# Performance work log

Hardware: AMD Instinct MI355X
Metric: run time of the kernel (lower is better)

Reference implementation:

```python
import jax, jax.numpy as jnp
import numpy as np

N_HEADS = 8
HEAD_DIM = 32
KSIZE = 3
IN_CH = 128
OUT_CH = 256


def setup_inputs() -> dict:
    key = jax.random.key(0)
    k1, k2, k3, k4 = jax.random.split(key, 4)
    x = jax.random.normal(k1, (8, IN_CH, 64, 64), dtype=jnp.float32)
    w_key = jax.random.normal(k2, (N_HEADS * HEAD_DIM, IN_CH), dtype=jnp.float32) * 0.05
    b_key = jax.random.normal(k3, (N_HEADS * HEAD_DIM,), dtype=jnp.float32) * 0.05
    # memory init in torch: uniform in [-1, 1)
    memory = jax.random.uniform(k4, (N_HEADS, HEAD_DIM * KSIZE * KSIZE, OUT_CH // N_HEADS),
                                dtype=jnp.float32) * 2.0 - 1.0
    return {"x": x, "w_key": w_key, "b_key": b_key, "memory": memory}


def _unfold(z, k):
    # z: [b, C, Hp, Wp] padded; returns [b, C*k*k, H*W] with torch.unfold layout
    b, C, Hp, Wp = z.shape
    H, W = Hp - k + 1, Wp - k + 1
    patches = [z[:, :, i:i + H, j:j + W] for i in range(k) for j in range(k)]
    # stack -> [b, C, k*k, H, W]; channel-major like torch unfold (C outer, kh*k+kw inner)
    p = jnp.stack(patches, axis=2)
    return p.reshape(b, C * k * k, H * W)


def reference(x, w_key, b_key, memory):
    b, c_in, H, W = x.shape
    k = KSIZE
    m = N_HEADS
    # 1x1 conv (to_mem_key)
    key_map = jnp.einsum('oi,bihw->bohw', w_key, x) + b_key[None, :, None, None]
    # ZeroPad2d((k//2, k%2, k//2, k%2)) = (left, right, top, bottom)
    pl, pr = k // 2, k % 2
    padded = jnp.pad(key_map, ((0, 0), (0, 0), (pl, pr), (pl, pr)))
    unf = _unfold(padded, k)                      # [b, C*k*k, L], C = m*head_dim
    ckk = unf.shape[1]
    L = unf.shape[2]
    c = ckk // m
    # rearrange 'b (c m) l -> b m c l' (m is the FAST factor, per einops pattern)
    attn = unf.reshape(b, c, m, L).transpose(0, 2, 1, 3)   # [b, m, c, L]
    attn = jax.nn.softmax(attn, axis=2)
    out = jnp.einsum('nki,bnkl->bnil', memory, attn)       # [b, m, head_out, L]
    # rearrange 'b m c (h w) -> b (m c) h w'
    return out.reshape(b, m * out.shape[2], H, W)
```

## Files before the change

### kernel.cpp

```cpp
#include <hip/hip_runtime.h>
#include <hip/hip_bf16.h>

#define B_   8
#define CIN  128
#define CKEY 256
#define NH   8
#define HOUT 32
#define CPH  288
#define HW   4096

#define ESTR   264
#define EROW   (66 * ESTR)
#define E2_BYTES   (4 * EROW * 2)
#define XBUF_BYTES (64 * 136 * 2)
#define SMEM_BYTES (E2_BYTES + XBUF_BYTES)

typedef __attribute__((ext_vector_type(8))) short bf16x8;
typedef __attribute__((ext_vector_type(4))) float f32x4;

static __device__ __forceinline__ unsigned bfpack2(float a, float b) {
  __hip_bfloat162 h = __float22bfloat162_rn(float2{a, b});
  unsigned r;
  __builtin_memcpy(&r, &h, 4);
  return r;
}

__global__ __launch_bounds__(512, 2) void fused_kernel(
    const float* __restrict__ x, const float* __restrict__ wk,
    const float* __restrict__ mem, const float* __restrict__ bk,
    float* __restrict__ out)
{
  extern __shared__ char smem[];
  unsigned short* e2 = (unsigned short*)smem;
  unsigned*       xdw = (unsigned*)(smem + E2_BYTES);

  const int tid = threadIdx.x;
  const int bid = blockIdx.x;
  const int b  = bid & 7;
  const int h0 = (bid >> 3) * 2;
  const int lane = tid & 63;
  const int wv = __builtin_amdgcn_readfirstlane(tid >> 6);
  const int li = lane & 15, q = lane >> 4;

  float bias[2][4];
#pragma unroll
  for (int sh = 0; sh < 2; ++sh)
#pragma unroll
    for (int r = 0; r < 4; ++r)
      bias[sh][r] = bk[wv + 8 * (sh * 16 + 4 * q + r)];

  const int spx = tid & 63, sicg = tid >> 6;
  const int sxor = ((spx >> 3) & 7) << 3;

  const bool valid[4] = {h0 - 1 >= 0, true, true, h0 + 2 < 64};
  unsigned pk[4][8];
#pragma unroll
  for (int r = 0; r < 4; ++r) {
    if (!valid[r]) continue;
    const int y = h0 - 1 + r;
    const float* xr = x + (size_t)b * CIN * HW + y * 64 + spx;
#pragma unroll
    for (int r4 = 0; r4 < 4; ++r4) {
      const int ic0 = 4 * sicg + 32 * r4;
      const float v0 = xr[(size_t)(ic0 + 0) * HW];
      const float v1 = xr[(size_t)(ic0 + 1) * HW];
      const float v2 = xr[(size_t)(ic0 + 2) * HW];
      const float v3 = xr[(size_t)(ic0 + 3) * HW];
      pk[r][2 * r4 + 0] = bfpack2(v0, v1);
      pk[r][2 * r4 + 1] = bfpack2(v2, v3);
    }
  }

  bf16x8 wf[2][4];
#pragma unroll
  for (int sh = 0; sh < 2; ++sh)
#pragma unroll
    for (int ks = 0; ks < 4; ++ks) {
      const int och = wv + 8 * (sh * 16 + li);
      const float* src = wk + (size_t)och * CIN + ks * 32 + q * 8;
      const float4 v0 = *(const float4*)(src);
      const float4 v1 = *(const float4*)(src + 4);
      const int4 piv = make_int4(bfpack2(v0.x, v0.y), bfpack2(v0.z, v0.w),
                                 bfpack2(v1.x, v1.y), bfpack2(v1.z, v1.w));
      wf[sh][ks] = __builtin_bit_cast(bf16x8, piv);
    }

  bf16x8 mfr[9][2];
#pragma unroll
  for (int p = 0; p < 9; ++p) {
    const int cb = (wv - p + 8) & 7;
#pragma unroll
    for (int ib = 0; ib < 2; ++ib) {
      const int i = ib * 16 + li;
      unsigned pr[4];
#pragma unroll
      for (int jj = 0; jj < 4; ++jj) {
        const int s0 = q * 8 + 2 * jj;
        const int c0 = cb + 8 * s0;
        const int c1 = cb + 8 * (s0 + 1);
        const int t0 = (9 * c0 + p) >> 3;
        const int t1 = (9 * c1 + p) >> 3;
        const float f0 = mem[((size_t)wv * CPH + t0) * HOUT + i];
        const float f1 = mem[((size_t)wv * CPH + t1) * HOUT + i];
        pr[jj] = bfpack2(f0, f1);
      }
      mfr[p][ib] = __builtin_bit_cast(bf16x8, make_int4(pr[0], pr[1], pr[2], pr[3]));
    }
  }

#pragma unroll
  for (int r = 0; r < 4; r += 3) {
    if (!valid[r]) {
      unsigned* erow = (unsigned*)(e2 + r * EROW);
      for (int d = tid; d < 66 * 132; d += 512) erow[d] = 0x3F803F80u;
    }
  }

#pragma unroll
  for (int rr = 0; rr < 4; ++rr) {
    if (valid[rr]) {
#pragma unroll
      for (int r4 = 0; r4 < 4; ++r4) {
        const int o = (2 * sicg + 16 * r4) ^ sxor;
        *(uint2*)(xdw + spx * 68 + o) = make_uint2(pk[rr][2 * r4], pk[rr][2 * r4 + 1]);
      }
    }
    __syncthreads();
    if (valid[rr]) {
      f32x4 acc[2][4];
#pragma unroll
      for (int sh = 0; sh < 2; ++sh)
#pragma unroll
        for (int pt = 0; pt < 4; ++pt) {
          f32x4 cv; cv[0] = bias[sh][0]; cv[1] = bias[sh][1];
          cv[2] = bias[sh][2]; cv[3] = bias[sh][3];
          acc[sh][pt] = cv;
        }
#pragma unroll
      for (int ks = 0; ks < 4; ++ks) {
        const bf16x8 a0 = wf[0][ks];
        const bf16x8 a1 = wf[1][ks];
#pragma unroll
        for (int pt = 0; pt < 4; ++pt) {
          const int px  = pt * 16 + li;
          const int blk = (ks * 16 + q * 4) ^ (((px >> 3) & 7) << 3);
          const bf16x8 bfr = *(const bf16x8*)(xdw + px * 68 + blk);
          acc[0][pt] = __builtin_amdgcn_mfma_f32_16x16x32_bf16(a0, bfr, acc[0][pt], 0, 0, 0);
          acc[1][pt] = __builtin_amdgcn_mfma_f32_16x16x32_bf16(a1, bfr, acc[1][pt], 0, 0, 0);
        }
      }
      unsigned short* erow = e2 + rr * EROW;
#pragma unroll
      for (int sh = 0; sh < 2; ++sh)
#pragma unroll
        for (int pt = 0; pt < 4; ++pt) {
          const float w0 = __expf(acc[sh][pt][0]);
          const float w1 = __expf(acc[sh][pt][1]);
          const float w2 = __expf(acc[sh][pt][2]);
          const float w3 = __expf(acc[sh][pt][3]);
          unsigned short* dst = erow + (pt * 16 + li + 1) * ESTR
                              + wv * 32 + sh * 16 + 4 * q;
          *(uint2*)dst = make_uint2(bfpack2(w0, w1), bfpack2(w2, w3));
        }
      if (tid < 256) {
        const int xcol = (tid & 1) ? 65 : 0;
        ((unsigned*)(erow + xcol * ESTR))[tid >> 1] = 0x3F803F80u;
      }
    }
    __syncthreads();
  }

  const int m = wv;
  const int4 onesi = make_int4(0x3F803F80, 0x3F803F80, 0x3F803F80, 0x3F803F80);
  const bf16x8 bones = __builtin_bit_cast(bf16x8, onesi);

#pragma unroll
  for (int hh = 0; hh < 2; ++hh) {
    f32x4 acc[4][2], accs[4];
#pragma unroll
    for (int pb = 0; pb < 4; ++pb) {
      acc[pb][0] = {0.f, 0.f, 0.f, 0.f};
      acc[pb][1] = {0.f, 0.f, 0.f, 0.f};
      accs[pb]   = {0.f, 0.f, 0.f, 0.f};
    }
#pragma unroll
    for (int p = 0; p < 9; ++p) {
      const bf16x8 bm0 = mfr[p][0];
      const bf16x8 bm1 = mfr[p][1];
      const int cm   = (m - p + 8) & 7;
      const int rrow = hh + p / 3;
      const int dxp  = p - 3 * (p / 3);
      const unsigned short* abase = e2 + rrow * EROW + (li + dxp) * ESTR
                                  + cm * 32 + q * 8;
#pragma unroll
      for (int pb = 0; pb < 4; ++pb) {
        const bf16x8 af = *(const bf16x8*)(abase + pb * 16 * ESTR);
        acc[pb][0] = __builtin_amdgcn_mfma_f32_16x16x32_bf16(bm0, af, acc[pb][0], 0, 0, 0);
        acc[pb][1] = __builtin_amdgcn_mfma_f32_16x16x32_bf16(bm1, af, acc[pb][1], 0, 0, 0);
        accs[pb]   = __builtin_amdgcn_mfma_f32_16x16x32_bf16(bones, af, accs[pb], 0, 0, 0);
      }
    }
    float* ob = out + ((size_t)(b * CKEY + m * HOUT)) * HW + (h0 + hh) * 64;
#pragma unroll
    for (int pb = 0; pb < 4; ++pb) {
      const float inv = 1.0f / accs[pb][0];
#pragma unroll
      for (int n = 0; n < 2; ++n)
#pragma unroll
        for (int r = 0; r < 4; ++r)
          ob[(size_t)(n * 16 + 4 * q + r) * HW + pb * 16 + li] =
              acc[pb][n][r] * inv;
    }
  }
}

extern "C" void kernel_launch(void* const* d_in, const int* in_sizes, int n_in,
                              void* d_out, int out_size, void* d_ws, size_t ws_size,
                              hipStream_t stream) {
  const float* x   = (const float*)d_in[0];
  const float* wk  = (const float*)d_in[1];
  const float* bk  = (const float*)d_in[2];
  const float* mem = (const float*)d_in[3];
  (void)d_ws; (void)ws_size;

  (void)hipFuncSetAttribute((const void*)fused_kernel,
                            hipFuncAttributeMaxDynamicSharedMemorySize, SMEM_BYTES);

  fused_kernel<<<dim3(256), dim3(512), SMEM_BYTES, stream>>>(
      x, wk, mem, bk, (float*)d_out);
}
```

Baseline: 110.9 us.

## Split fused kernel into conv+exp kernel and attention kernel via global workspace

Replaces the single fused kernel, which recomputed the 1x1 conv for halo rows (4 rows per 2 output rows), with two kernels. The first computes exp(conv) for each row once into a padded bf16 global buffer and also prepacks the memory MFMA fragments. The second reads the three neighbouring rows from global memory to do the softmax-weighted aggregation, one output row per block. This removes the duplicated conv work and the large LDS footprint, at the cost of an extra launch and a global round trip of about 17 MB of bf16 intermediates.

```diff
diff --git a/kernel.cpp b/kernel.cpp
--- a/kernel.cpp
+++ b/kernel.cpp
@@ -9,11 +9,11 @@
 #define CPH  288
 #define HW   4096
 
-#define ESTR   264
-#define EROW   (66 * ESTR)
-#define E2_BYTES   (4 * EROW * 2)
-#define XBUF_BYTES (64 * 136 * 2)
-#define SMEM_BYTES (E2_BYTES + XBUF_BYTES)
+#define EPX   256
+#define EROWG (66 * EPX)
+#define EBATG (66 * EROWG)
+#define E_BYTES   ((size_t)B_ * EBATG * 2)
+#define MFRAG_OFF E_BYTES
 
 typedef __attribute__((ext_vector_type(8))) short bf16x8;
 typedef __attribute__((ext_vector_type(4))) float f32x4;
@@ -24,23 +24,46 @@
   __builtin_memcpy(&r, &h, 4);
   return r;
 }
-
-__global__ __launch_bounds__(512, 2) void fused_kernel(
+static __device__ __forceinline__ unsigned short f2bf(float f) {
+  unsigned u = __builtin_bit_cast(unsigned, f);
+  u += 0x7FFFu + ((u >> 16) & 1u);
+  return (unsigned short)(u >> 16);
+}
+
+__global__ __launch_bounds__(512, 2) void conv_kernel(
     const float* __restrict__ x, const float* __restrict__ wk,
-    const float* __restrict__ mem, const float* __restrict__ bk,
-    float* __restrict__ out)
+    const float* __restrict__ bk, const float* __restrict__ mem,
+    unsigned short* __restrict__ EG, unsigned short* __restrict__ mfragP)
 {
-  extern __shared__ char smem[];
-  unsigned short* e2 = (unsigned short*)smem;
-  unsigned*       xdw = (unsigned*)(smem + E2_BYTES);
-
+  __shared__ unsigned xdw[64 * 68];
   const int tid = threadIdx.x;
-  const int bid = blockIdx.x;
-  const int b  = bid & 7;
-  const int h0 = (bid >> 3) * 2;
+  const int gb = blockIdx.x;
+
+  if (gb >= 512) {
+    const int idx  = (gb - 512) * 512 + tid;
+    const int lane = idx & 63, fi = idx >> 6;
+    const int ib = fi & 1, pm = fi >> 1;
+    const int p = pm % 9, mh = pm / 9;
+    const int li = lane & 15, q = lane >> 4;
+    const int i = ib * 16 + li;
+    unsigned short* dst = mfragP + (size_t)idx * 8;
+#pragma unroll
+    for (int j = 0; j < 8; ++j) {
+      const int s = q * 8 + j;
+      const int c = ((mh - p + 8) & 7) + 8 * s;
+      const int t = (9 * c + p) >> 3;
+      dst[j] = f2bf(mem[((size_t)mh * CPH + t) * HOUT + i]);
+    }
+    return;
+  }
+
+  const int b = gb & 7;
+  const int y = gb >> 3;
   const int lane = tid & 63;
   const int wv = __builtin_amdgcn_readfirstlane(tid >> 6);
   const int li = lane & 15, q = lane >> 4;
+  const int spx = tid & 63, sicg = tid >> 6;
+  const int sxor = ((spx >> 3) & 7) << 3;
 
   float bias[2][4];
 #pragma unroll
@@ -49,26 +72,17 @@
     for (int r = 0; r < 4; ++r)
       bias[sh][r] = bk[wv + 8 * (sh * 16 + 4 * q + r)];
 
-  const int spx = tid & 63, sicg = tid >> 6;
-  const int sxor = ((spx >> 3) & 7) << 3;
-
-  const bool valid[4] = {h0 - 1 >= 0, true, true, h0 + 2 < 64};
-  unsigned pk[4][8];
-#pragma unroll
-  for (int r = 0; r < 4; ++r) {
-    if (!valid[r]) continue;
-    const int y = h0 - 1 + r;
-    const float* xr = x + (size_t)b * CIN * HW + y * 64 + spx;
-#pragma unroll
-    for (int r4 = 0; r4 < 4; ++r4) {
-      const int ic0 = 4 * sicg + 32 * r4;
-      const float v0 = xr[(size_t)(ic0 + 0) * HW];
-      const float v1 = xr[(size_t)(ic0 + 1) * HW];
-      const float v2 = xr[(size_t)(ic0 + 2) * HW];
-      const float v3 = xr[(size_t)(ic0 + 3) * HW];
-      pk[r][2 * r4 + 0] = bfpack2(v0, v1);
-      pk[r][2 * r4 + 1] = bfpack2(v2, v3);
-    }
+  unsigned pk[8];
+  const float* xr = x + (size_t)b * CIN * HW + y * 64 + spx;
+#pragma unroll
+  for (int r4 = 0; r4 < 4; ++r4) {
+    const int ic0 = 4 * sicg + 32 * r4;
+    const float v0 = xr[(size_t)(ic0 + 0) * HW];
+    const float v1 = xr[(size_t)(ic0 + 1) * HW];
+    const float v2 = xr[(size_t)(ic0 + 2) * HW];
+    const float v3 = xr[(size_t)(ic0 + 3) * HW];
+    pk[2 * r4 + 0] = bfpack2(v0, v1);
+    pk[2 * r4 + 1] = bfpack2(v2, v3);
   }
 
   bf16x8 wf[2][4];
@@ -85,132 +99,117 @@
       wf[sh][ks] = __builtin_bit_cast(bf16x8, piv);
     }
 
-  bf16x8 mfr[9][2];
-#pragma unroll
-  for (int p = 0; p < 9; ++p) {
-    const int cb = (wv - p + 8) & 7;
-#pragma unroll
-    for (int ib = 0; ib < 2; ++ib) {
-      const int i = ib * 16 + li;
-      unsigned pr[4];
-#pragma unroll
-      for (int jj = 0; jj < 4; ++jj) {
-        const int s0 = q * 8 + 2 * jj;
-        const int c0 = cb + 8 * s0;
-        const int c1 = cb + 8 * (s0 + 1);
-        const int t0 = (9 * c0 + p) >> 3;
-        const int t1 = (9 * c1 + p) >> 3;
-        const float f0 = mem[((size_t)wv * CPH + t0) * HOUT + i];
-        const float f1 = mem[((size_t)wv * CPH + t1) * HOUT + i];
-        pr[jj] = bfpack2(f0, f1);
-      }
-      mfr[p][ib] = __builtin_bit_cast(bf16x8, make_int4(pr[0], pr[1], pr[2], pr[3]));
-    }
-  }
-
-#pragma unroll
-  for (int r = 0; r < 4; r += 3) {
-    if (!valid[r]) {
-      unsigned* erow = (unsigned*)(e2 + r * EROW);
-      for (int d = tid; d < 66 * 132; d += 512) erow[d] = 0x3F803F80u;
-    }
-  }
-
-#pragma unroll
-  for (int rr = 0; rr < 4; ++rr) {
-    if (valid[rr]) {
-#pragma unroll
-      for (int r4 = 0; r4 < 4; ++r4) {
-        const int o = (2 * sicg + 16 * r4) ^ sxor;
-        *(uint2*)(xdw + spx * 68 + o) = make_uint2(pk[rr][2 * r4], pk[rr][2 * r4 + 1]);
-      }
-    }
-    __syncthreads();
-    if (valid[rr]) {
-      f32x4 acc[2][4];
-#pragma unroll
-      for (int sh = 0; sh < 2; ++sh)
-#pragma unroll
-        for (int pt = 0; pt < 4; ++pt) {
-          f32x4 cv; cv[0] = bias[sh][0]; cv[1] = bias[sh][1];
-          cv[2] = bias[sh][2]; cv[3] = bias[sh][3];
-          acc[sh][pt] = cv;
-        }
-#pragma unroll
-      for (int ks = 0; ks < 4; ++ks) {
-        const bf16x8 a0 = wf[0][ks];
-        const bf16x8 a1 = wf[1][ks];
-#pragma unroll
-        for (int pt = 0; pt < 4; ++pt) {
-          const int px  = pt * 16 + li;
-          const int blk = (ks * 16 + q * 4) ^ (((px >> 3) & 7) << 3);
-          const bf16x8 bfr = *(const bf16x8*)(xdw + px * 68 + blk);
-          acc[0][pt] = __builtin_amdgcn_mfma_f32_16x16x32_bf16(a0, bfr, acc[0][pt], 0, 0, 0);
-          acc[1][pt] = __builtin_amdgcn_mfma_f32_16x16x32_bf16(a1, bfr, acc[1][pt], 0, 0, 0);
-        }
-      }
-      unsigned short* erow = e2 + rr * EROW;
-#pragma unroll
-      for (int sh = 0; sh < 2; ++sh)
-#pragma unroll
-        for (int pt = 0; pt < 4; ++pt) {
-          const float w0 = __expf(acc[sh][pt][0]);
-          const float w1 = __expf(acc[sh][pt][1]);
-          const float w2 = __expf(acc[sh][pt][2]);
-          const float w3 = __expf(acc[sh][pt][3]);
-          unsigned short* dst = erow + (pt * 16 + li + 1) * ESTR
-                              + wv * 32 + sh * 16 + 4 * q;
-          *(uint2*)dst = make_uint2(bfpack2(w0, w1), bfpack2(w2, w3));
-        }
-      if (tid < 256) {
-        const int xcol = (tid & 1) ? 65 : 0;
-        ((unsigned*)(erow + xcol * ESTR))[tid >> 1] = 0x3F803F80u;
-      }
-    }
-    __syncthreads();
-  }
-
-  const int m = wv;
+#pragma unroll
+  for (int r4 = 0; r4 < 4; ++r4) {
+    const int o = (2 * sicg + 16 * r4) ^ sxor;
+    *(uint2*)(xdw + spx * 68 + o) = make_uint2(pk[2 * r4], pk[2 * r4 + 1]);
+  }
+  __syncthreads();
+
+  f32x4 acc[2][4];
+#pragma unroll
+  for (int sh = 0; sh < 2; ++sh)
+#pragma unroll
+    for (int pt = 0; pt < 4; ++pt) {
+      f32x4 cv; cv[0] = bias[sh][0]; cv[1] = bias[sh][1];
+      cv[2] = bias[sh][2]; cv[3] = bias[sh][3];
+      acc[sh][pt] = cv;
+    }
+#pragma unroll
+  for (int ks = 0; ks < 4; ++ks) {
+    const bf16x8 a0 = wf[0][ks];
+    const bf16x8 a1 = wf[1][ks];
+#pragma unroll
+    for (int pt = 0; pt < 4; ++pt) {
+      const int px  = pt * 16 + li;
+      const int blk = (ks * 16 + q * 4) ^ (((px >> 3) & 7) << 3);
+      const bf16x8 bfr = *(const bf16x8*)(xdw + px * 68 + blk);
+      acc[0][pt] = __builtin_amdgcn_mfma_f32_16x16x32_bf16(a0, bfr, acc[0][pt], 0, 0, 0);
+      acc[1][pt] = __builtin_amdgcn_mfma_f32_16x16x32_bf16(a1, bfr, acc[1][pt], 0, 0, 0);
+    }
+  }
+
+  unsigned short* erow = EG + (size_t)(b * 66 + y + 1) * EROWG;
+#pragma unroll
+  for (int sh = 0; sh < 2; ++sh)
+#pragma unroll
+    for (int pt = 0; pt < 4; ++pt) {
+      const float w0 = __expf(acc[sh][pt][0]);
+      const float w1 = __expf(acc[sh][pt][1]);
+      const float w2 = __expf(acc[sh][pt][2]);
+      const float w3 = __expf(acc[sh][pt][3]);
+      unsigned short* dst = erow + (size_t)(pt * 16 + li + 1) * EPX
+                          + wv * 32 + sh * 16 + 4 * q;
+      *(uint2*)dst = make_uint2(bfpack2(w0, w1), bfpack2(w2, w3));
+    }
+
+  unsigned* rowdw = (unsigned*)erow;
+  if (tid < 256) {
+    const int c = tid & 127;
+    if (tid < 128) rowdw[c] = 0x3F803F80u;
+    else           rowdw[65 * 128 + c] = 0x3F803F80u;
+  }
+  if (y == 0) {
+    unsigned* r0 = (unsigned*)(EG + (size_t)(b * 66 + 0) * EROWG);
+    for (int d = tid; d < 66 * 128; d += 512) r0[d] = 0x3F803F80u;
+  }
+  if (y == 63) {
+    unsigned* r65 = (unsigned*)(EG + (size_t)(b * 66 + 65) * EROWG);
+    for (int d = tid; d < 66 * 128; d += 512) r65[d] = 0x3F803F80u;
+  }
+}
+
+__global__ __launch_bounds__(512, 2) void attn_kernel(
+    const unsigned short* __restrict__ EG,
+    const unsigned short* __restrict__ mfragP,
+    float* __restrict__ out)
+{
+  const int tid = threadIdx.x, bid = blockIdx.x;
+  const int b = bid & 7, h = bid >> 3;
+  const int lane = tid & 63;
+  const int m = __builtin_amdgcn_readfirstlane(tid >> 6);
+  const int li = lane & 15, q = lane >> 4;
+
+  const unsigned short* mf = mfragP + (size_t)(m * 9) * 2 * 64 * 8;
   const int4 onesi = make_int4(0x3F803F80, 0x3F803F80, 0x3F803F80, 0x3F803F80);
   const bf16x8 bones = __builtin_bit_cast(bf16x8, onesi);
 
-#pragma unroll
-  for (int hh = 0; hh < 2; ++hh) {
-    f32x4 acc[4][2], accs[4];
+  f32x4 acc[4][2], accs[4];
+#pragma unroll
+  for (int pb = 0; pb < 4; ++pb) {
+    acc[pb][0] = {0.f, 0.f, 0.f, 0.f};
+    acc[pb][1] = {0.f, 0.f, 0.f, 0.f};
+    accs[pb]   = {0.f, 0.f, 0.f, 0.f};
+  }
+
+#pragma unroll
+  for (int p = 0; p < 9; ++p) {
+    const bf16x8 bm0 = *(const bf16x8*)(mf + ((size_t)((p * 2 + 0) * 64 + lane)) * 8);
+    const bf16x8 bm1 = *(const bf16x8*)(mf + ((size_t)((p * 2 + 1) * 64 + lane)) * 8);
+    const int cm  = (m - p + 8) & 7;
+    const int ry  = h + p / 3;
+    const int dxp = p - 3 * (p / 3);
+    const unsigned short* abase = EG + (size_t)(b * 66 + ry) * EROWG
+                                + (size_t)(li + dxp) * EPX + cm * 32 + q * 8;
 #pragma unroll
     for (int pb = 0; pb < 4; ++pb) {
-      acc[pb][0] = {0.f, 0.f, 0.f, 0.f};
-      acc[pb][1] = {0.f, 0.f, 0.f, 0.f};
-      accs[pb]   = {0.f, 0.f, 0.f, 0.f};
-    }
-#pragma unroll
-    for (int p = 0; p < 9; ++p) {
-      const bf16x8 bm0 = mfr[p][0];
-      const bf16x8 bm1 = mfr[p][1];
-      const int cm   = (m - p + 8) & 7;
-      const int rrow = hh + p / 3;
-      const int dxp  = p - 3 * (p / 3);
-      const unsigned short* abase = e2 + rrow * EROW + (li + dxp) * ESTR
-                                  + cm * 32 + q * 8;
-#pragma unroll
-      for (int pb = 0; pb < 4; ++pb) {
-        const bf16x8 af = *(const bf16x8*)(abase + pb * 16 * ESTR);
-        acc[pb][0] = __builtin_amdgcn_mfma_f32_16x16x32_bf16(bm0, af, acc[pb][0], 0, 0, 0);
-        acc[pb][1] = __builtin_amdgcn_mfma_f32_16x16x32_bf16(bm1, af, acc[pb][1], 0, 0, 0);
-        accs[pb]   = __builtin_amdgcn_mfma_f32_16x16x32_bf16(bones, af, accs[pb], 0, 0, 0);
-      }
-    }
-    float* ob = out + ((size_t)(b * CKEY + m * HOUT)) * HW + (h0 + hh) * 64;
-#pragma unroll
-    for (int pb = 0; pb < 4; ++pb) {
-      const float inv = 1.0f / accs[pb][0];
-#pragma unroll
-      for (int n = 0; n < 2; ++n)
-#pragma unroll
-        for (int r = 0; r < 4; ++r)
-          ob[(size_t)(n * 16 + 4 * q + r) * HW + pb * 16 + li] =
-              acc[pb][n][r] * inv;
-    }
+      const bf16x8 af = *(const bf16x8*)(abase + (size_t)pb * 16 * EPX);
+      acc[pb][0] = __builtin_amdgcn_mfma_f32_16x16x32_bf16(bm0, af, acc[pb][0], 0, 0, 0);
+      acc[pb][1] = __builtin_amdgcn_mfma_f32_16x16x32_bf16(bm1, af, acc[pb][1], 0, 0, 0);
+      accs[pb]   = __builtin_amdgcn_mfma_f32_16x16x32_bf16(bones, af, accs[pb], 0, 0, 0);
+    }
+  }
+
+  float* ob = out + ((size_t)(b * CKEY + m * HOUT)) * HW + h * 64;
+#pragma unroll
+  for (int pb = 0; pb < 4; ++pb) {
+    const float inv = 1.0f / accs[pb][0];
+#pragma unroll
+    for (int n = 0; n < 2; ++n)
+#pragma unroll
+      for (int r = 0; r < 4; ++r)
+        ob[(size_t)(n * 16 + 4 * q + r) * HW + pb * 16 + li] =
+            acc[pb][n][r] * inv;
   }
 }
 
@@ -221,11 +220,10 @@
   const float* wk  = (const float*)d_in[1];
   const float* bk  = (const float*)d_in[2];
   const float* mem = (const float*)d_in[3];
-  (void)d_ws; (void)ws_size;
-
-  (void)hipFuncSetAttribute((const void*)fused_kernel,
-                            hipFuncAttributeMaxDynamicSharedMemorySize, SMEM_BYTES);
-
-  fused_kernel<<<dim3(256), dim3(512), SMEM_BYTES, stream>>>(
-      x, wk, mem, bk, (float*)d_out);
-}
+
+  unsigned short* EG     = (unsigned short*)d_ws;
+  unsigned short* mfragP = (unsigned short*)((char*)d_ws + MFRAG_OFF);
+
+  conv_kernel<<<dim3(530), dim3(512), 0, stream>>>(x, wk, bk, mem, EG, mfragP);
+  attn_kernel<<<dim3(512), dim3(512), 0, stream>>>(EG, mfragP, (float*)d_out);
+}
```

New measurement: 111.9 us. About the same (+0.9%).

## Use 1024-thread blocks splitting heads/rows across waves and prepack memory fragments

Applied to the files above, without the earlier changes.

Doubles the block size to 16 waves so each wave handles one head and one half (key-map channel half, then one output row), halving per-wave register state. The memory-matrix bf16 MFMA fragments are built once by a small prep kernel into workspace, so each block no longer gathers and converts them with scattered loads. This adds a second kernel launch and global fragment loads in the main loop. Occupancy changes from two 512-thread blocks per CU to one 1024-thread block.

```diff
diff --git a/kernel.cpp b/kernel.cpp
--- a/kernel.cpp
+++ b/kernel.cpp
@@ -24,10 +24,34 @@
   __builtin_memcpy(&r, &h, 4);
   return r;
 }
-
-__global__ __launch_bounds__(512, 2) void fused_kernel(
+static __device__ __forceinline__ unsigned short f2bf(float f) {
+  unsigned u = __builtin_bit_cast(unsigned, f);
+  u += 0x7FFFu + ((u >> 16) & 1u);
+  return (unsigned short)(u >> 16);
+}
+
+__global__ __launch_bounds__(256) void prep_kernel(
+    const float* __restrict__ mem, unsigned short* __restrict__ mfragP)
+{
+  const int idx  = blockIdx.x * 256 + threadIdx.x;
+  const int lane = idx & 63, fi = idx >> 6;
+  const int ib = fi & 1, pm = fi >> 1;
+  const int p = pm % 9, m = pm / 9;
+  const int li = lane & 15, q = lane >> 4;
+  const int i = ib * 16 + li;
+  unsigned short* dst = mfragP + (size_t)idx * 8;
+#pragma unroll
+  for (int j = 0; j < 8; ++j) {
+    const int s = q * 8 + j;
+    const int c = ((m - p + 8) & 7) + 8 * s;
+    const int t = (9 * c + p) >> 3;
+    dst[j] = f2bf(mem[((size_t)m * CPH + t) * HOUT + i]);
+  }
+}
+
+__global__ __launch_bounds__(1024) void fused_kernel(
     const float* __restrict__ x, const float* __restrict__ wk,
-    const float* __restrict__ mem, const float* __restrict__ bk,
+    const unsigned short* __restrict__ mfragP, const float* __restrict__ bk,
     float* __restrict__ out)
 {
   extern __shared__ char smem[];
@@ -40,79 +64,53 @@
   const int h0 = (bid >> 3) * 2;
   const int lane = tid & 63;
   const int wv = __builtin_amdgcn_readfirstlane(tid >> 6);
+  const int cm = wv & 7, sh = wv >> 3;
   const int li = lane & 15, q = lane >> 4;
 
-  float bias[2][4];
-#pragma unroll
-  for (int sh = 0; sh < 2; ++sh)
-#pragma unroll
-    for (int r = 0; r < 4; ++r)
-      bias[sh][r] = bk[wv + 8 * (sh * 16 + 4 * q + r)];
-
-  const int spx = tid & 63, sicg = tid >> 6;
+  float bias[4];
+#pragma unroll
+  for (int r = 0; r < 4; ++r)
+    bias[r] = bk[cm + 8 * (sh * 16 + 4 * q + r)];
+
+  const int spx = tid & 63, g = tid >> 6;
   const int sxor = ((spx >> 3) & 7) << 3;
 
   const bool valid[4] = {h0 - 1 >= 0, true, true, h0 + 2 < 64};
-  unsigned pk[4][8];
+  unsigned pk[4][4];
 #pragma unroll
   for (int r = 0; r < 4; ++r) {
     if (!valid[r]) continue;
     const int y = h0 - 1 + r;
     const float* xr = x + (size_t)b * CIN * HW + y * 64 + spx;
 #pragma unroll
-    for (int r4 = 0; r4 < 4; ++r4) {
-      const int ic0 = 4 * sicg + 32 * r4;
+    for (int r2 = 0; r2 < 2; ++r2) {
+      const int ic0 = 4 * g + 64 * r2;
       const float v0 = xr[(size_t)(ic0 + 0) * HW];
       const float v1 = xr[(size_t)(ic0 + 1) * HW];
       const float v2 = xr[(size_t)(ic0 + 2) * HW];
       const float v3 = xr[(size_t)(ic0 + 3) * HW];
-      pk[r][2 * r4 + 0] = bfpack2(v0, v1);
-      pk[r][2 * r4 + 1] = bfpack2(v2, v3);
-    }
-  }
-
-  bf16x8 wf[2][4];
-#pragma unroll
-  for (int sh = 0; sh < 2; ++sh)
-#pragma unroll
-    for (int ks = 0; ks < 4; ++ks) {
-      const int och = wv + 8 * (sh * 16 + li);
-      const float* src = wk + (size_t)och * CIN + ks * 32 + q * 8;
-      const float4 v0 = *(const float4*)(src);
-      const float4 v1 = *(const float4*)(src + 4);
-      const int4 piv = make_int4(bfpack2(v0.x, v0.y), bfpack2(v0.z, v0.w),
-                                 bfpack2(v1.x, v1.y), bfpack2(v1.z, v1.w));
-      wf[sh][ks] = __builtin_bit_cast(bf16x8, piv);
-    }
-
-  bf16x8 mfr[9][2];
-#pragma unroll
-  for (int p = 0; p < 9; ++p) {
-    const int cb = (wv - p + 8) & 7;
-#pragma unroll
-    for (int ib = 0; ib < 2; ++ib) {
-      const int i = ib * 16 + li;
-      unsigned pr[4];
-#pragma unroll
-      for (int jj = 0; jj < 4; ++jj) {
-        const int s0 = q * 8 + 2 * jj;
-        const int c0 = cb + 8 * s0;
-        const int c1 = cb + 8 * (s0 + 1);
-        const int t0 = (9 * c0 + p) >> 3;
-        const int t1 = (9 * c1 + p) >> 3;
-        const float f0 = mem[((size_t)wv * CPH + t0) * HOUT + i];
-        const float f1 = mem[((size_t)wv * CPH + t1) * HOUT + i];
-        pr[jj] = bfpack2(f0, f1);
-      }
-      mfr[p][ib] = __builtin_bit_cast(bf16x8, make_int4(pr[0], pr[1], pr[2], pr[3]));
-    }
+      pk[r][2 * r2 + 0] = bfpack2(v0, v1);
+      pk[r][2 * r2 + 1] = bfpack2(v2, v3);
+    }
+  }
+
+  bf16x8 wf[4];
+#pragma unroll
+  for (int ks = 0; ks < 4; ++ks) {
+    const int och = cm + 8 * (sh * 16 + li);
+    const float* src = wk + (size_t)och * CIN + ks * 32 + q * 8;
+    const float4 v0 = *(const float4*)(src);
+    const float4 v1 = *(const float4*)(src + 4);
+    const int4 piv = make_int4(bfpack2(v0.x, v0.y), bfpack2(v0.z, v0.w),
+                               bfpack2(v1.x, v1.y), bfpack2(v1.z, v1.w));
+    wf[ks] = __builtin_bit_cast(bf16x8, piv);
   }
 
 #pragma unroll
   for (int r = 0; r < 4; r += 3) {
     if (!valid[r]) {
       unsigned* erow = (unsigned*)(e2 + r * EROW);
-      for (int d = tid; d < 66 * 132; d += 512) erow[d] = 0x3F803F80u;
+      for (int d = tid; d < 66 * 132; d += 1024) erow[d] = 0x3F803F80u;
     }
   }
 
@@ -120,48 +118,42 @@
   for (int rr = 0; rr < 4; ++rr) {
     if (valid[rr]) {
 #pragma unroll
-      for (int r4 = 0; r4 < 4; ++r4) {
-        const int o = (2 * sicg + 16 * r4) ^ sxor;
-        *(uint2*)(xdw + spx * 68 + o) = make_uint2(pk[rr][2 * r4], pk[rr][2 * r4 + 1]);
+      for (int r2 = 0; r2 < 2; ++r2) {
+        const int o = (2 * g + 32 * r2) ^ sxor;
+        *(uint2*)(xdw + spx * 68 + o) = make_uint2(pk[rr][2 * r2], pk[rr][2 * r2 + 1]);
       }
     }
     __syncthreads();
     if (valid[rr]) {
-      f32x4 acc[2][4];
-#pragma unroll
-      for (int sh = 0; sh < 2; ++sh)
-#pragma unroll
-        for (int pt = 0; pt < 4; ++pt) {
-          f32x4 cv; cv[0] = bias[sh][0]; cv[1] = bias[sh][1];
-          cv[2] = bias[sh][2]; cv[3] = bias[sh][3];
-          acc[sh][pt] = cv;
-        }
+      f32x4 acc[4];
+#pragma unroll
+      for (int pt = 0; pt < 4; ++pt) {
+        f32x4 cv; cv[0] = bias[0]; cv[1] = bias[1];
+        cv[2] = bias[2]; cv[3] = bias[3];
+        acc[pt] = cv;
+      }
 #pragma unroll
       for (int ks = 0; ks < 4; ++ks) {
-        const bf16x8 a0 = wf[0][ks];
-        const bf16x8 a1 = wf[1][ks];
+        const bf16x8 a0 = wf[ks];
 #pragma unroll
         for (int pt = 0; pt < 4; ++pt) {
           const int px  = pt * 16 + li;
           const int blk = (ks * 16 + q * 4) ^ (((px >> 3) & 7) << 3);
           const bf16x8 bfr = *(const bf16x8*)(xdw + px * 68 + blk);
-          acc[0][pt] = __builtin_amdgcn_mfma_f32_16x16x32_bf16(a0, bfr, acc[0][pt], 0, 0, 0);
-          acc[1][pt] = __builtin_amdgcn_mfma_f32_16x16x32_bf16(a1, bfr, acc[1][pt], 0, 0, 0);
+          acc[pt] = __builtin_amdgcn_mfma_f32_16x16x32_bf16(a0, bfr, acc[pt], 0, 0, 0);
         }
       }
       unsigned short* erow = e2 + rr * EROW;
 #pragma unroll
-      for (int sh = 0; sh < 2; ++sh)
-#pragma unroll
-        for (int pt = 0; pt < 4; ++pt) {
-          const float w0 = __expf(acc[sh][pt][0]);
-          const float w1 = __expf(acc[sh][pt][1]);
-          const float w2 = __expf(acc[sh][pt][2]);
-          const float w3 = __expf(acc[sh][pt][3]);
-          unsigned short* dst = erow + (pt * 16 + li + 1) * ESTR
-                              + wv * 32 + sh * 16 + 4 * q;
-          *(uint2*)dst = make_uint2(bfpack2(w0, w1), bfpack2(w2, w3));
-        }
+      for (int pt = 0; pt < 4; ++pt) {
+        const float w0 = __expf(acc[pt][0]);
+        const float w1 = __expf(acc[pt][1]);
+        const float w2 = __expf(acc[pt][2]);
+        const float w3 = __expf(acc[pt][3]);
+        unsigned short* dst = erow + (pt * 16 + li + 1) * ESTR
+                            + cm * 32 + sh * 16 + 4 * q;
+        *(uint2*)dst = make_uint2(bfpack2(w0, w1), bfpack2(w2, w3));
+      }
       if (tid < 256) {
         const int xcol = (tid & 1) ? 65 : 0;
         ((unsigned*)(erow + xcol * ESTR))[tid >> 1] = 0x3F803F80u;
@@ -170,47 +162,45 @@
     __syncthreads();
   }
 
-  const int m = wv;
+  const int m = cm, hh = sh;
+  const unsigned short* mf = mfragP + (size_t)(m * 9) * 2 * 64 * 8;
   const int4 onesi = make_int4(0x3F803F80, 0x3F803F80, 0x3F803F80, 0x3F803F80);
   const bf16x8 bones = __builtin_bit_cast(bf16x8, onesi);
 
-#pragma unroll
-  for (int hh = 0; hh < 2; ++hh) {
-    f32x4 acc[4][2], accs[4];
+  f32x4 acc[4][2], accs[4];
+#pragma unroll
+  for (int pb = 0; pb < 4; ++pb) {
+    acc[pb][0] = {0.f, 0.f, 0.f, 0.f};
+    acc[pb][1] = {0.f, 0.f, 0.f, 0.f};
+    accs[pb]   = {0.f, 0.f, 0.f, 0.f};
+  }
+#pragma unroll
+  for (int p = 0; p < 9; ++p) {
+    const bf16x8 bm0 = *(const bf16x8*)(mf + ((size_t)((p * 2 + 0) * 64 + lane)) * 8);
+    const bf16x8 bm1 = *(const bf16x8*)(mf + ((size_t)((p * 2 + 1) * 64 + lane)) * 8);
+    const int cmp  = (m - p + 8) & 7;
+    const int rrow = hh + p / 3;
+    const int dxp  = p - 3 * (p / 3);
+    const unsigned short* abase = e2 + rrow * EROW + (li + dxp) * ESTR
+                                + cmp * 32 + q * 8;
 #pragma unroll
     for (int pb = 0; pb < 4; ++pb) {
-      acc[pb][0] = {0.f, 0.f, 0.f, 0.f};
-      acc[pb][1] = {0.f, 0.f, 0.f, 0.f};
-      accs[pb]   = {0.f, 0.f, 0.f, 0.f};
-    }
-#pragma unroll
-    for (int p = 0; p < 9; ++p) {
-      const bf16x8 bm0 = mfr[p][0];
-      const bf16x8 bm1 = mfr[p][1];
-      const int cm   = (m - p + 8) & 7;
-      const int rrow = hh + p / 3;
-      const int dxp  = p - 3 * (p / 3);
-      const unsigned short* abase = e2 + rrow * EROW + (li + dxp) * ESTR
-                                  + cm * 32 + q * 8;
-#pragma unroll
-      for (int pb = 0; pb < 4; ++pb) {
-        const bf16x8 af = *(const bf16x8*)(abase + pb * 16 * ESTR);
-        acc[pb][0] = __builtin_amdgcn_mfma_f32_16x16x32_bf16(bm0, af, acc[pb][0], 0, 0, 0);
-        acc[pb][1] = __builtin_amdgcn_mfma_f32_16x16x32_bf16(bm1, af, acc[pb][1], 0, 0, 0);
-        accs[pb]   = __builtin_amdgcn_mfma_f32_16x16x32_bf16(bones, af, accs[pb], 0, 0, 0);
-      }
-    }
-    float* ob = out + ((size_t)(b * CKEY + m * HOUT)) * HW + (h0 + hh) * 64;
-#pragma unroll
-    for (int pb = 0; pb < 4; ++pb) {
-      const float inv = 1.0f / accs[pb][0];
-#pragma unroll
-      for (int n = 0; n < 2; ++n)
-#pragma unroll
-        for (int r = 0; r < 4; ++r)
-          ob[(size_t)(n * 16 + 4 * q + r) * HW + pb * 16 + li] =
-              acc[pb][n][r] * inv;
-    }
+      const bf16x8 af = *(const bf16x8*)(abase + pb * 16 * ESTR);
+      acc[pb][0] = __builtin_amdgcn_mfma_f32_16x16x32_bf16(bm0, af, acc[pb][0], 0, 0, 0);
+      acc[pb][1] = __builtin_amdgcn_mfma_f32_16x16x32_bf16(bm1, af, acc[pb][1], 0, 0, 0);
+      accs[pb]   = __builtin_amdgcn_mfma_f32_16x16x32_bf16(bones, af, accs[pb], 0, 0, 0);
+    }
+  }
+  float* ob = out + ((size_t)(b * CKEY + m * HOUT)) * HW + (h0 + hh) * 64;
+#pragma unroll
+  for (int pb = 0; pb < 4; ++pb) {
+    const float inv = 1.0f / accs[pb][0];
+#pragma unroll
+    for (int n = 0; n < 2; ++n)
+#pragma unroll
+      for (int r = 0; r < 4; ++r)
+        ob[(size_t)(n * 16 + 4 * q + r) * HW + pb * 16 + li] =
+            acc[pb][n][r] * inv;
   }
 }
 
@@ -221,11 +211,13 @@
   const float* wk  = (const float*)d_in[1];
   const float* bk  = (const float*)d_in[2];
   const float* mem = (const float*)d_in[3];
-  (void)d_ws; (void)ws_size;
+
+  unsigned short* mfragP = (unsigned short*)d_ws;
 
   (void)hipFuncSetAttribute((const void*)fused_kernel,
                             hipFuncAttributeMaxDynamicSharedMemorySize, SMEM_BYTES);
 
-  fused_kernel<<<dim3(256), dim3(512), SMEM_BYTES, stream>>>(
-      x, wk, mem, bk, (float*)d_out);
-}
+  prep_kernel<<<dim3(36), dim3(256), 0, stream>>>(mem, mfragP);
+  fused_kernel<<<dim3(256), dim3(1024), SMEM_BYTES, stream>>>(
+      x, wk, mfragP, bk, (float*)d_out);
+}
```

Result: faster. 94.53 us (-14.8%).

## Precompute memory fragments in a prep kernel and alias x buffer with exp tile

Applied to the files above, without the earlier changes.

Adds a small prep kernel that converts the memory tensor to bf16 in MFMA fragment order in workspace, so the main kernel loads fragments per use instead of holding 18 fragments in registers. The x staging buffer now aliases the exp tile in shared memory, and all four rows' 1x1-conv MFMAs run in one pass with fewer barriers. The intent is to cut register pressure and LDS footprint. It adds a second launch, more global loads inside the hot loop, and drops the min-blocks launch bound while keeping 4x2x4 accumulators live.

```diff
diff --git a/kernel.cpp b/kernel.cpp
--- a/kernel.cpp
+++ b/kernel.cpp
@@ -12,8 +12,8 @@
 #define ESTR   264
 #define EROW   (66 * ESTR)
 #define E2_BYTES   (4 * EROW * 2)
-#define XBUF_BYTES (64 * 136 * 2)
-#define SMEM_BYTES (E2_BYTES + XBUF_BYTES)
+#define XROW_DW    (64 * 68)
+#define SMEM_BYTES E2_BYTES
 
 typedef __attribute__((ext_vector_type(8))) short bf16x8;
 typedef __attribute__((ext_vector_type(4))) float f32x4;
@@ -24,15 +24,39 @@
   __builtin_memcpy(&r, &h, 4);
   return r;
 }
-
-__global__ __launch_bounds__(512, 2) void fused_kernel(
+static __device__ __forceinline__ unsigned short f2bf(float f) {
+  unsigned u = __builtin_bit_cast(unsigned, f);
+  u += 0x7FFFu + ((u >> 16) & 1u);
+  return (unsigned short)(u >> 16);
+}
+
+__global__ __launch_bounds__(256) void prep_kernel(
+    const float* __restrict__ mem, unsigned short* __restrict__ mfragP)
+{
+  const int idx  = blockIdx.x * 256 + threadIdx.x;
+  const int lane = idx & 63, fi = idx >> 6;
+  const int ib = fi & 1, pm = fi >> 1;
+  const int p = pm % 9, m = pm / 9;
+  const int li = lane & 15, q = lane >> 4;
+  const int i = ib * 16 + li;
+  unsigned short* dst = mfragP + (size_t)idx * 8;
+#pragma unroll
+  for (int j = 0; j < 8; ++j) {
+    const int s = q * 8 + j;
+    const int c = ((m - p + 8) & 7) + 8 * s;
+    const int t = (9 * c + p) >> 3;
+    dst[j] = f2bf(mem[((size_t)m * CPH + t) * HOUT + i]);
+  }
+}
+
+__global__ __launch_bounds__(512) void fused_kernel(
     const float* __restrict__ x, const float* __restrict__ wk,
-    const float* __restrict__ mem, const float* __restrict__ bk,
+    const unsigned short* __restrict__ mfragP, const float* __restrict__ bk,
     float* __restrict__ out)
 {
   extern __shared__ char smem[];
   unsigned short* e2 = (unsigned short*)smem;
-  unsigned*       xdw = (unsigned*)(smem + E2_BYTES);
+  unsigned*       xdw = (unsigned*)smem;
 
   const int tid = threadIdx.x;
   const int bid = blockIdx.x;
@@ -85,29 +109,69 @@
       wf[sh][ks] = __builtin_bit_cast(bf16x8, piv);
     }
 
-  bf16x8 mfr[9][2];
-#pragma unroll
-  for (int p = 0; p < 9; ++p) {
-    const int cb = (wv - p + 8) & 7;
-#pragma unroll
-    for (int ib = 0; ib < 2; ++ib) {
-      const int i = ib * 16 + li;
-      unsigned pr[4];
-#pragma unroll
-      for (int jj = 0; jj < 4; ++jj) {
-        const int s0 = q * 8 + 2 * jj;
-        const int c0 = cb + 8 * s0;
-        const int c1 = cb + 8 * (s0 + 1);
-        const int t0 = (9 * c0 + p) >> 3;
-        const int t1 = (9 * c1 + p) >> 3;
-        const float f0 = mem[((size_t)wv * CPH + t0) * HOUT + i];
-        const float f1 = mem[((size_t)wv * CPH + t1) * HOUT + i];
-        pr[jj] = bfpack2(f0, f1);
-      }
-      mfr[p][ib] = __builtin_bit_cast(bf16x8, make_int4(pr[0], pr[1], pr[2], pr[3]));
-    }
-  }
-
+#pragma unroll
+  for (int rr = 0; rr < 4; ++rr) {
+    if (!valid[rr]) continue;
+#pragma unroll
+    for (int r4 = 0; r4 < 4; ++r4) {
+      const int o = (2 * sicg + 16 * r4) ^ sxor;
+      *(uint2*)(xdw + rr * XROW_DW + spx * 68 + o) =
+          make_uint2(pk[rr][2 * r4], pk[rr][2 * r4 + 1]);
+    }
+  }
+  __syncthreads();
+
+  f32x4 acc[4][2][4];
+#pragma unroll
+  for (int rr = 0; rr < 4; ++rr)
+#pragma unroll
+    for (int sh = 0; sh < 2; ++sh)
+#pragma unroll
+      for (int pt = 0; pt < 4; ++pt) {
+        f32x4 cv; cv[0] = bias[sh][0]; cv[1] = bias[sh][1];
+        cv[2] = bias[sh][2]; cv[3] = bias[sh][3];
+        acc[rr][sh][pt] = cv;
+      }
+#pragma unroll
+  for (int ks = 0; ks < 4; ++ks) {
+    const bf16x8 a0 = wf[0][ks];
+    const bf16x8 a1 = wf[1][ks];
+#pragma unroll
+    for (int rr = 0; rr < 4; ++rr) {
+      if (!valid[rr]) continue;
+#pragma unroll
+      for (int pt = 0; pt < 4; ++pt) {
+        const int px  = pt * 16 + li;
+        const int blk = (ks * 16 + q * 4) ^ (((px >> 3) & 7) << 3);
+        const bf16x8 bfr = *(const bf16x8*)(xdw + rr * XROW_DW + px * 68 + blk);
+        acc[rr][0][pt] = __builtin_amdgcn_mfma_f32_16x16x32_bf16(a0, bfr, acc[rr][0][pt], 0, 0, 0);
+        acc[rr][1][pt] = __builtin_amdgcn_mfma_f32_16x16x32_bf16(a1, bfr, acc[rr][1][pt], 0, 0, 0);
+      }
+    }
+  }
+  __syncthreads();
+
+#pragma unroll
+  for (int rr = 0; rr < 4; ++rr) {
+    if (!valid[rr]) continue;
+    unsigned short* erow = e2 + rr * EROW;
+#pragma unroll
+    for (int sh = 0; sh < 2; ++sh)
+#pragma unroll
+      for (int pt = 0; pt < 4; ++pt) {
+        const float w0 = __expf(acc[rr][sh][pt][0]);
+        const float w1 = __expf(acc[rr][sh][pt][1]);
+        const float w2 = __expf(acc[rr][sh][pt][2]);
+        const float w3 = __expf(acc[rr][sh][pt][3]);
+        unsigned short* dst = erow + (pt * 16 + li + 1) * ESTR
+                            + wv * 32 + sh * 16 + 4 * q;
+        *(uint2*)dst = make_uint2(bfpack2(w0, w1), bfpack2(w2, w3));
+      }
+    if (tid < 256) {
+      const int xcol = (tid & 1) ? 65 : 0;
+      ((unsigned*)(erow + xcol * ESTR))[tid >> 1] = 0x3F803F80u;
+    }
+  }
 #pragma unroll
   for (int r = 0; r < 4; r += 3) {
     if (!valid[r]) {
@@ -115,89 +179,37 @@
       for (int d = tid; d < 66 * 132; d += 512) erow[d] = 0x3F803F80u;
     }
   }
-
-#pragma unroll
-  for (int rr = 0; rr < 4; ++rr) {
-    if (valid[rr]) {
-#pragma unroll
-      for (int r4 = 0; r4 < 4; ++r4) {
-        const int o = (2 * sicg + 16 * r4) ^ sxor;
-        *(uint2*)(xdw + spx * 68 + o) = make_uint2(pk[rr][2 * r4], pk[rr][2 * r4 + 1]);
-      }
-    }
-    __syncthreads();
-    if (valid[rr]) {
-      f32x4 acc[2][4];
-#pragma unroll
-      for (int sh = 0; sh < 2; ++sh)
-#pragma unroll
-        for (int pt = 0; pt < 4; ++pt) {
-          f32x4 cv; cv[0] = bias[sh][0]; cv[1] = bias[sh][1];
-          cv[2] = bias[sh][2]; cv[3] = bias[sh][3];
-          acc[sh][pt] = cv;
-        }
-#pragma unroll
-      for (int ks = 0; ks < 4; ++ks) {
-        const bf16x8 a0 = wf[0][ks];
-        const bf16x8 a1 = wf[1][ks];
-#pragma unroll
-        for (int pt = 0; pt < 4; ++pt) {
-          const int px  = pt * 16 + li;
-          const int blk = (ks * 16 + q * 4) ^ (((px >> 3) & 7) << 3);
-          const bf16x8 bfr = *(const bf16x8*)(xdw + px * 68 + blk);
-          acc[0][pt] = __builtin_amdgcn_mfma_f32_16x16x32_bf16(a0, bfr, acc[0][pt], 0, 0, 0);
-          acc[1][pt] = __builtin_amdgcn_mfma_f32_16x16x32_bf16(a1, bfr, acc[1][pt], 0, 0, 0);
-        }
-      }
-      unsigned short* erow = e2 + rr * EROW;
-#pragma unroll
-      for (int sh = 0; sh < 2; ++sh)
-#pragma unroll
-        for (int pt = 0; pt < 4; ++pt) {
-          const float w0 = __expf(acc[sh][pt][0]);
-          const float w1 = __expf(acc[sh][pt][1]);
-          const float w2 = __expf(acc[sh][pt][2]);
-          const float w3 = __expf(acc[sh][pt][3]);
-          unsigned short* dst = erow + (pt * 16 + li + 1) * ESTR
-                              + wv * 32 + sh * 16 + 4 * q;
-          *(uint2*)dst = make_uint2(bfpack2(w0, w1), bfpack2(w2, w3));
-        }
-      if (tid < 256) {
-        const int xcol = (tid & 1) ? 65 : 0;
-        ((unsigned*)(erow + xcol * ESTR))[tid >> 1] = 0x3F803F80u;
-      }
-    }
-    __syncthreads();
-  }
+  __syncthreads();
 
   const int m = wv;
+  const unsigned short* mf = mfragP + (size_t)(m * 9) * 2 * 64 * 8;
   const int4 onesi = make_int4(0x3F803F80, 0x3F803F80, 0x3F803F80, 0x3F803F80);
   const bf16x8 bones = __builtin_bit_cast(bf16x8, onesi);
 
 #pragma unroll
   for (int hh = 0; hh < 2; ++hh) {
-    f32x4 acc[4][2], accs[4];
+    f32x4 acc2[4][2], accs[4];
 #pragma unroll
     for (int pb = 0; pb < 4; ++pb) {
-      acc[pb][0] = {0.f, 0.f, 0.f, 0.f};
-      acc[pb][1] = {0.f, 0.f, 0.f, 0.f};
-      accs[pb]   = {0.f, 0.f, 0.f, 0.f};
+      acc2[pb][0] = {0.f, 0.f, 0.f, 0.f};
+      acc2[pb][1] = {0.f, 0.f, 0.f, 0.f};
+      accs[pb]    = {0.f, 0.f, 0.f, 0.f};
     }
 #pragma unroll
     for (int p = 0; p < 9; ++p) {
-      const bf16x8 bm0 = mfr[p][0];
-      const bf16x8 bm1 = mfr[p][1];
-      const int cm   = (m - p + 8) & 7;
+      const bf16x8 bm0 = *(const bf16x8*)(mf + ((size_t)((p * 2 + 0) * 64 + lane)) * 8);
+      const bf16x8 bm1 = *(const bf16x8*)(mf + ((size_t)((p * 2 + 1) * 64 + lane)) * 8);
+      const int cmp  = (m - p + 8) & 7;
       const int rrow = hh + p / 3;
       const int dxp  = p - 3 * (p / 3);
       const unsigned short* abase = e2 + rrow * EROW + (li + dxp) * ESTR
-                                  + cm * 32 + q * 8;
+                                  + cmp * 32 + q * 8;
 #pragma unroll
       for (int pb = 0; pb < 4; ++pb) {
         const bf16x8 af = *(const bf16x8*)(abase + pb * 16 * ESTR);
-        acc[pb][0] = __builtin_amdgcn_mfma_f32_16x16x32_bf16(bm0, af, acc[pb][0], 0, 0, 0);
-        acc[pb][1] = __builtin_amdgcn_mfma_f32_16x16x32_bf16(bm1, af, acc[pb][1], 0, 0, 0);
-        accs[pb]   = __builtin_amdgcn_mfma_f32_16x16x32_bf16(bones, af, accs[pb], 0, 0, 0);
+        acc2[pb][0] = __builtin_amdgcn_mfma_f32_16x16x32_bf16(bm0, af, acc2[pb][0], 0, 0, 0);
+        acc2[pb][1] = __builtin_amdgcn_mfma_f32_16x16x32_bf16(bm1, af, acc2[pb][1], 0, 0, 0);
+        accs[pb]    = __builtin_amdgcn_mfma_f32_16x16x32_bf16(bones, af, accs[pb], 0, 0, 0);
       }
     }
     float* ob = out + ((size_t)(b * CKEY + m * HOUT)) * HW + (h0 + hh) * 64;
@@ -209,7 +221,7 @@
 #pragma unroll
         for (int r = 0; r < 4; ++r)
           ob[(size_t)(n * 16 + 4 * q + r) * HW + pb * 16 + li] =
-              acc[pb][n][r] * inv;
+              acc2[pb][n][r] * inv;
     }
   }
 }
@@ -221,11 +233,13 @@
   const float* wk  = (const float*)d_in[1];
   const float* bk  = (const float*)d_in[2];
   const float* mem = (const float*)d_in[3];
-  (void)d_ws; (void)ws_size;
+
+  unsigned short* mfragP = (unsigned short*)d_ws;
 
   (void)hipFuncSetAttribute((const void*)fused_kernel,
                             hipFuncAttributeMaxDynamicSharedMemorySize, SMEM_BYTES);
 
+  prep_kernel<<<dim3(36), dim3(256), 0, stream>>>(mem, mfragP);
   fused_kernel<<<dim3(256), dim3(512), SMEM_BYTES, stream>>>(
-      x, wk, mem, bk, (float*)d_out);
-}
+      x, wk, mfragP, bk, (float*)d_out);
+}
```

Measured after the change: 94.84 us. -14.5%, faster.
